# Kernel tuning notes

Measured on AMD Instinct MI355X. Metric: run time of the kernel, lower is better.

Reference implementation:

```python
import jax, jax.numpy as jnp
import numpy as np

B, T, C, H = 2, 2048, 1024, 16
D = C // H  # head_dim = 64

def setup_inputs() -> dict:
    key = jax.random.key(0)
    k1, k2, k3 = jax.random.split(key, 3)
    x = jax.random.normal(k1, (B, T, C), dtype=jnp.float32)
    W_qkv = jax.random.normal(k2, (C, 3 * C), dtype=jnp.float32) * (C ** -0.5)
    b_qkv = jnp.zeros((3 * C,), dtype=jnp.float32)
    W_proj = jax.random.normal(k3, (C, C), dtype=jnp.float32) * (C ** -0.5)
    b_proj = jnp.zeros((C,), dtype=jnp.float32)
    return {"x": x, "W_qkv": W_qkv, "b_qkv": b_qkv, "W_proj": W_proj, "b_proj": b_proj}

def reference(x, W_qkv, b_qkv, W_proj, b_proj):
    # qkv projection: [B,T,3C]
    qkv = jnp.einsum('btc,cf->btf', x, W_qkv) + b_qkv
    q, k, v = jnp.split(qkv, 3, axis=-1)
    # split heads -> [B,H,T,D]
    q = q.reshape(B, T, H, D).transpose(0, 2, 1, 3)
    k = k.reshape(B, T, H, D).transpose(0, 2, 1, 3)
    v = v.reshape(B, T, H, D).transpose(0, 2, 1, 3)
    scale = 1.0 / jnp.sqrt(jnp.float32(D))
    att = jnp.einsum('bhqd,bhkd->bhqk', q, k) * scale  # [B,H,T,T]
    causal = jnp.tril(jnp.ones((T, T), dtype=bool))
    att = jnp.where(causal[None, None, :, :], att, jnp.float32(-jnp.inf))
    att = jax.nn.softmax(att, axis=-1)
    y = jnp.einsum('bhqk,bhkd->bhqd', att, v)  # [B,H,T,D]
    y = y.transpose(0, 2, 1, 3).reshape(B, T, C)
    return jnp.einsum('btc,cf->btf', y, W_proj) + b_proj
```

## Files before the change

kernel.cpp:

```cpp
#include <hip/hip_runtime.h>
#include <hip/hip_bf16.h>

#define Bq 2
#define Tq 2048
#define Cq 1024
#define Hq 16
#define Dq 64
#define Mq (Bq * Tq)

typedef __bf16 bf16x8 __attribute__((ext_vector_type(8)));
typedef float f32x4 __attribute__((ext_vector_type(4)));
typedef unsigned short u16;

static __device__ __forceinline__ u16 f2bf(float f) {
  union { float f; unsigned u; } v; v.f = f;
  return (u16)((v.u + 0x7fffu + ((v.u >> 16) & 1u)) >> 16);
}

static __device__ __forceinline__ f32x4 mfma16(bf16x8 a, bf16x8 b, f32x4 c) {
  return __builtin_amdgcn_mfma_f32_16x16x32_bf16(a, b, c, 0, 0, 0);
}

#define GLD16(g, l)                                                   \
  __builtin_amdgcn_global_load_lds(                                   \
      (const __attribute__((address_space(1))) unsigned int*)(g),     \
      (__attribute__((address_space(3))) unsigned int*)(l), 16, 0, 0)

static __device__ __forceinline__ int swz(int col, int row) {
  return (col & 7) + 8 * (((col >> 3) ^ (row >> 3)) & 7);
}

__global__ __launch_bounds__(256) void convert_x(const float* __restrict__ x,
                                                 u16* __restrict__ xb) {
  int i = (blockIdx.x * 256 + threadIdx.x) * 8;
  float4 a = *(const float4*)(x + i);
  float4 b = *(const float4*)(x + i + 4);
  u16 tmp[8];
  tmp[0] = f2bf(a.x); tmp[1] = f2bf(a.y); tmp[2] = f2bf(a.z); tmp[3] = f2bf(a.w);
  tmp[4] = f2bf(b.x); tmp[5] = f2bf(b.y); tmp[6] = f2bf(b.z); tmp[7] = f2bf(b.w);
  *(uint4*)(xb + i) = *(const uint4*)tmp;
}

__global__ __launch_bounds__(256) void transpose_w(const float* __restrict__ W,
                                                   u16* __restrict__ Wt,
                                                   int K, int N) {
  __shared__ __align__(16) u16 Ts[64][72];
  const int k0 = blockIdx.x * 64, n0 = blockIdx.y * 64;
  const int t = threadIdx.x;
  const int r = t >> 2, c0 = (t & 3) * 16;
  const float* src = W + (size_t)(k0 + r) * N + n0 + c0;
  u16 v16[16];
#pragma unroll
  for (int i = 0; i < 4; i++) {
    float4 f = *(const float4*)(src + 4 * i);
    v16[4 * i + 0] = f2bf(f.x); v16[4 * i + 1] = f2bf(f.y);
    v16[4 * i + 2] = f2bf(f.z); v16[4 * i + 3] = f2bf(f.w);
  }
#pragma unroll
  for (int j = 0; j < 16; j++) Ts[c0 + j][r] = v16[j];
  __syncthreads();
  u16* dst = Wt + (size_t)(n0 + r) * K + k0 + c0;
  *(uint4*)dst = *(const uint4*)&Ts[r][c0];
  *(uint4*)(dst + 8) = *(const uint4*)&Ts[r][c0 + 8];
}

__global__ __launch_bounds__(256) void qkv_gemm(
    const u16* __restrict__ A, const u16* __restrict__ Bt,
    const float* __restrict__ bias,
    u16* __restrict__ qw, u16* __restrict__ kw, u16* __restrict__ vw) {
  const int K = 1024;
  __shared__ __align__(16) u16 As[128][32];
  __shared__ __align__(16) u16 Bs[128][32];
  const int m0 = blockIdx.x * 128, n0 = blockIdx.y * 128;
  const int t = threadIdx.x, lane = t & 63, w = t >> 6;
  const int wm = (w >> 1) * 64, wn = (w & 1) * 64;
  const int l15 = lane & 15, l4 = lane >> 4;
  const int lr = lane >> 2, lc = (lane & 3) * 8;
  f32x4 acc[4][4] = {};
  const u16* ga = A + (size_t)(m0 + w * 16 + lr) * K + lc;
  const u16* gb = Bt + (size_t)(n0 + w * 16 + lr) * K + lc;

  for (int kk = 0; kk < K; kk += 32) {
    __syncthreads();
    GLD16(ga + kk, &As[w * 16][0]);
    GLD16(ga + (size_t)64 * K + kk, &As[64 + w * 16][0]);
    GLD16(gb + kk, &Bs[w * 16][0]);
    GLD16(gb + (size_t)64 * K + kk, &Bs[64 + w * 16][0]);
    __syncthreads();
    bf16x8 af[4], bfr[4];
#pragma unroll
    for (int i = 0; i < 4; i++) {
      af[i] = *(const bf16x8*)&As[wm + i * 16 + l15][l4 * 8];
      bfr[i] = *(const bf16x8*)&Bs[wn + i * 16 + l15][l4 * 8];
    }
#pragma unroll
    for (int mi = 0; mi < 4; mi++)
#pragma unroll
      for (int ni = 0; ni < 4; ni++)
        acc[mi][ni] = mfma16(af[mi], bfr[ni], acc[mi][ni]);
  }
#pragma unroll
  for (int mi = 0; mi < 4; mi++) {
#pragma unroll
    for (int ni = 0; ni < 4; ni++) {
#pragma unroll
      for (int r = 0; r < 4; r++) {
        int row = m0 + wm + mi * 16 + l4 * 4 + r;
        int col = n0 + wn + ni * 16 + l15;
        float val = acc[mi][ni][r] + bias[col];
        int which = col >> 10, c = col & 1023;
        int h = c >> 6, d = c & 63;
        int b = row >> 11, tt = row & 2047;
        u16* dst = (which == 0) ? qw : ((which == 1) ? kw : vw);
        dst[(size_t)((b * Hq + h) * Tq + tt) * Dq + d] = f2bf(val);
      }
    }
  }
}

__global__ __launch_bounds__(256) void attn(
    const u16* __restrict__ qw, const u16* __restrict__ kw,
    const u16* __restrict__ vw, u16* __restrict__ yw) {
  const int bh = blockIdx.x;
  const int qy = blockIdx.y;
  const int qb = (qy < 8) ? (15 - qy) : (qy - 8);
  __shared__ __align__(16) u16 Ks[64][72];
  __shared__ __align__(16) u16 Vt[64][72];
  __shared__ __align__(16) u16 Ps[128][72];
  const int t = threadIdx.x, lane = t & 63, w = t >> 6;
  const int l15 = lane & 15, l4 = lane >> 4;
  const size_t base = (size_t)bh * Tq * Dq;
  const int rr = t >> 2, d0 = (t & 3) * 16;

  bf16x8 qf[2][2];
  {
    const u16* qp = qw + base + (size_t)(qb * 128 + w * 32) * Dq;
#pragma unroll
    for (int s = 0; s < 2; s++)
#pragma unroll
      for (int h = 0; h < 2; h++)
        qf[s][h] = *(const bf16x8*)(qp + (size_t)(s * 16 + l15) * Dq + h * 32 + l4 * 8);
  }

  float m[2][4], lsum[2][4];
  f32x4 accO[2][4] = {};
#pragma unroll
  for (int s = 0; s < 2; s++)
#pragma unroll
    for (int r = 0; r < 4; r++) { m[s][r] = -1e30f; lsum[s][r] = 0.f; }

  const float kscale = 0.125f * 1.44269504088896340736f;
  const int kvmax = 2 * qb + 1;

  const u16* ksrc = kw + base + (size_t)rr * Dq + d0;
  const u16* vsrc = vw + base + (size_t)rr * Dq + d0;
  uint4 kreg0 = *(const uint4*)ksrc, kreg1 = *(const uint4*)(ksrc + 8);
  uint4 vreg0 = *(const uint4*)vsrc, vreg1 = *(const uint4*)(vsrc + 8);

  for (int kv = 0; kv <= kvmax; kv++) {
    __syncthreads();
    *(uint4*)&Ks[rr][d0] = kreg0;
    *(uint4*)&Ks[rr][d0 + 8] = kreg1;
    {
      union { uint4 q[2]; u16 s[16]; } vu;
      vu.q[0] = vreg0; vu.q[1] = vreg1;
#pragma unroll
      for (int j = 0; j < 16; j++) {
        int row = d0 + j;
        Vt[row][swz(rr, row)] = vu.s[j];
      }
    }
    if (kv < kvmax) {
      ksrc += 64 * Dq; vsrc += 64 * Dq;
      kreg0 = *(const uint4*)ksrc; kreg1 = *(const uint4*)(ksrc + 8);
      vreg0 = *(const uint4*)vsrc; vreg1 = *(const uint4*)(vsrc + 8);
    }
    __syncthreads();

    f32x4 sc[2][4];
    __builtin_amdgcn_s_setprio(1);
#pragma unroll
    for (int ct = 0; ct < 4; ct++) {
      bf16x8 kf0 = *(const bf16x8*)&Ks[ct * 16 + l15][l4 * 8];
      bf16x8 kf1 = *(const bf16x8*)&Ks[ct * 16 + l15][32 + l4 * 8];
      f32x4 z0 = {}; z0 = mfma16(qf[0][0], kf0, z0); z0 = mfma16(qf[0][1], kf1, z0);
      sc[0][ct] = z0;
      f32x4 z1 = {}; z1 = mfma16(qf[1][0], kf0, z1); z1 = mfma16(qf[1][1], kf1, z1);
      sc[1][ct] = z1;
    }
    __builtin_amdgcn_s_setprio(0);

    if (kv >= 2 * qb) {
#pragma unroll
      for (int s = 0; s < 2; s++)
#pragma unroll
        for (int ct = 0; ct < 4; ct++)
#pragma unroll
          for (int r = 0; r < 4; r++) {
            int q = qb * 128 + w * 32 + s * 16 + l4 * 4 + r;
            int k = kv * 64 + ct * 16 + l15;
            sc[s][ct][r] = (k > q) ? -1e30f : sc[s][ct][r] * kscale;
          }
    } else {
#pragma unroll
      for (int s = 0; s < 2; s++)
#pragma unroll
        for (int ct = 0; ct < 4; ct++)
#pragma unroll
          for (int r = 0; r < 4; r++) sc[s][ct][r] *= kscale;
    }

#pragma unroll
    for (int s = 0; s < 2; s++) {
      float corr[4], psum[4];
#pragma unroll
      for (int r = 0; r < 4; r++) {
        float v = fmaxf(fmaxf(sc[s][0][r], sc[s][1][r]),
                        fmaxf(sc[s][2][r], sc[s][3][r]));
#pragma unroll
        for (int off = 1; off < 16; off <<= 1) v = fmaxf(v, __shfl_xor(v, off));
        float mn = fmaxf(m[s][r], v);
        corr[r] = exp2f(m[s][r] - mn);
        m[s][r] = mn;
        psum[r] = 0.f;
      }
#pragma unroll
      for (int ct = 0; ct < 4; ct++)
#pragma unroll
        for (int r = 0; r < 4; r++) {
          float p = exp2f(sc[s][ct][r] - m[s][r]);
          psum[r] += p;
          int R = w * 32 + s * 16 + l4 * 4 + r;
          Ps[R][swz(ct * 16 + l15, R)] = f2bf(p);
        }
#pragma unroll
      for (int r = 0; r < 4; r++) {
        float v = psum[r];
#pragma unroll
        for (int off = 1; off < 16; off <<= 1) v += __shfl_xor(v, off);
        lsum[s][r] = lsum[s][r] * corr[r] + v;
      }
#pragma unroll
      for (int dt = 0; dt < 4; dt++)
#pragma unroll
        for (int r = 0; r < 4; r++) accO[s][dt][r] *= corr[r];
    }

    bf16x8 pf[2][2];
#pragma unroll
    for (int s = 0; s < 2; s++) {
      int R = w * 32 + s * 16 + l15;
      int e = (R >> 3) & 7;
      pf[s][0] = *(const bf16x8*)&Ps[R][8 * ((l4 ^ e) & 7)];
      pf[s][1] = *(const bf16x8*)&Ps[R][8 * (((4 + l4) ^ e) & 7)];
    }
    __builtin_amdgcn_s_setprio(1);
#pragma unroll
    for (int dt = 0; dt < 4; dt++) {
      int Rv = dt * 16 + l15;
      int ev = (Rv >> 3) & 7;
      bf16x8 vf0 = *(const bf16x8*)&Vt[Rv][8 * ((l4 ^ ev) & 7)];
      bf16x8 vf1 = *(const bf16x8*)&Vt[Rv][8 * (((4 + l4) ^ ev) & 7)];
      accO[0][dt] = mfma16(pf[0][0], vf0, accO[0][dt]);
      accO[0][dt] = mfma16(pf[0][1], vf1, accO[0][dt]);
      accO[1][dt] = mfma16(pf[1][0], vf0, accO[1][dt]);
      accO[1][dt] = mfma16(pf[1][1], vf1, accO[1][dt]);
    }
    __builtin_amdgcn_s_setprio(0);
  }

  const int b = bh >> 4, hd = bh & 15;
#pragma unroll
  for (int s = 0; s < 2; s++)
#pragma unroll
    for (int r = 0; r < 4; r++) {
      float inv = 1.0f / lsum[s][r];
      int tt = qb * 128 + w * 32 + s * 16 + l4 * 4 + r;
      size_t rowbase = ((size_t)(b * Tq + tt)) * Cq + hd * 64;
#pragma unroll
      for (int dt = 0; dt < 4; dt++)
        yw[rowbase + dt * 16 + l15] = f2bf(accO[s][dt][r] * inv);
    }
}

__global__ __launch_bounds__(256) void proj_gemm(
    const u16* __restrict__ A, const u16* __restrict__ Bt,
    const float* __restrict__ bias, float* __restrict__ out) {
  const int K = 1024, N = 1024;
  __shared__ __align__(16) u16 As[128][32];
  __shared__ __align__(16) u16 Bs[128][32];
  const int m0 = blockIdx.x * 128, n0 = blockIdx.y * 128;
  const int t = threadIdx.x, lane = t & 63, w = t >> 6;
  const int wm = (w >> 1) * 64, wn = (w & 1) * 64;
  const int l15 = lane & 15, l4 = lane >> 4;
  const int lr = lane >> 2, lc = (lane & 3) * 8;
  f32x4 acc[4][4] = {};
  const u16* ga = A + (size_t)(m0 + w * 16 + lr) * K + lc;
  const u16* gb = Bt + (size_t)(n0 + w * 16 + lr) * K + lc;

  for (int kk = 0; kk < K; kk += 32) {
    __syncthreads();
    GLD16(ga + kk, &As[w * 16][0]);
    GLD16(ga + (size_t)64 * K + kk, &As[64 + w * 16][0]);
    GLD16(gb + kk, &Bs[w * 16][0]);
    GLD16(gb + (size_t)64 * K + kk, &Bs[64 + w * 16][0]);
    __syncthreads();
    bf16x8 af[4], bfr[4];
#pragma unroll
    for (int i = 0; i < 4; i++) {
      af[i] = *(const bf16x8*)&As[wm + i * 16 + l15][l4 * 8];
      bfr[i] = *(const bf16x8*)&Bs[wn + i * 16 + l15][l4 * 8];
    }
#pragma unroll
    for (int mi = 0; mi < 4; mi++)
#pragma unroll
      for (int ni = 0; ni < 4; ni++)
        acc[mi][ni] = mfma16(af[mi], bfr[ni], acc[mi][ni]);
  }
#pragma unroll
  for (int mi = 0; mi < 4; mi++) {
#pragma unroll
    for (int ni = 0; ni < 4; ni++) {
#pragma unroll
      for (int r = 0; r < 4; r++) {
        int row = m0 + wm + mi * 16 + l4 * 4 + r;
        int col = n0 + wn + ni * 16 + l15;
        out[(size_t)row * N + col] = acc[mi][ni][r] + bias[col];
      }
    }
  }
}

extern "C" void kernel_launch(void* const* d_in, const int* in_sizes, int n_in,
                              void* d_out, int out_size, void* d_ws, size_t ws_size,
                              hipStream_t stream) {
  const float* x = (const float*)d_in[0];
  const float* W_qkv = (const float*)d_in[1];
  const float* b_qkv = (const float*)d_in[2];
  const float* W_proj = (const float*)d_in[3];
  const float* b_proj = (const float*)d_in[4];
  float* out = (float*)d_out;

  const size_t qkv_elems = (size_t)Bq * Hq * Tq * Dq;
  u16* qw = (u16*)d_ws;
  u16* kw = qw + qkv_elems;
  u16* vw = kw + qkv_elems;
  u16* xb = vw + qkv_elems;
  u16* wt = xb + (size_t)Mq * Cq;

  convert_x<<<dim3((Mq * Cq) / (256 * 8)), 256, 0, stream>>>(x, xb);
  transpose_w<<<dim3(Cq / 64, 3 * Cq / 64), 256, 0, stream>>>(W_qkv, wt, Cq, 3 * Cq);
  qkv_gemm<<<dim3(Mq / 128, 3 * Cq / 128), 256, 0, stream>>>(xb, wt, b_qkv, qw, kw, vw);
  transpose_w<<<dim3(Cq / 64, Cq / 64), 256, 0, stream>>>(W_proj, wt, Cq, Cq);
  u16* yw = xb;
  attn<<<dim3(Bq * Hq, Tq / 128), 256, 0, stream>>>(qw, kw, vw, yw);
  proj_gemm<<<dim3(Mq / 128, Cq / 128), 256, 0, stream>>>(yw, wt, b_proj, out);
}
```

Before: 249.5 us.

## Restructure attention to transposed S tiles with register-resident P and lazy rescale

The attention kernel now runs 512 threads, each wave owning 16 query rows instead of 32. It computes S^T (K as the A operand) so each lane holds one query column, and moves P into the PV MFMA operand layout with shuffles, which removes the Ps shared-memory round trip. The softmax scale is folded into Q in the QKV GEMM epilogue. Waves skip KV tiles that are fully masked for their rows, and the running max is only rescaled when it grows by more than a threshold. The costs are extra cross-lane shuffles, more waves contending for the shared K/V tiles, and lazy max updates that could reduce numerical headroom.

Result: faster. 207.3 us (-16.9%).

```diff
diff --git a/kernel.cpp b/kernel.cpp
--- a/kernel.cpp
+++ b/kernel.cpp
@@ -109,6 +109,7 @@
         int col = n0 + wn + ni * 16 + l15;
         float val = acc[mi][ni][r] + bias[col];
         int which = col >> 10, c = col & 1023;
+        if (which == 0) val *= 0.18033688011112042f;
         int h = c >> 6, d = c & 63;
         int b = row >> 11, tt = row & 2047;
         u16* dst = (which == 0) ? qw : ((which == 1) ? kw : vw);
@@ -118,7 +119,7 @@
   }
 }
 
-__global__ __launch_bounds__(256) void attn(
+__global__ __launch_bounds__(512, 4) void attn(
     const u16* __restrict__ qw, const u16* __restrict__ kw,
     const u16* __restrict__ vw, u16* __restrict__ yw) {
   const int bh = blockIdx.x;
@@ -126,161 +127,144 @@
   const int qb = (qy < 8) ? (15 - qy) : (qy - 8);
   __shared__ __align__(16) u16 Ks[64][72];
   __shared__ __align__(16) u16 Vt[64][72];
-  __shared__ __align__(16) u16 Ps[128][72];
   const int t = threadIdx.x, lane = t & 63, w = t >> 6;
   const int l15 = lane & 15, l4 = lane >> 4;
   const size_t base = (size_t)bh * Tq * Dq;
-  const int rr = t >> 2, d0 = (t & 3) * 16;
-
-  bf16x8 qf[2][2];
+  const int rv = t >> 3, c8 = t & 7;
+
+  const int qs = qb * 128 + w * 16;
+  bf16x8 qf[2];
   {
-    const u16* qp = qw + base + (size_t)(qb * 128 + w * 32) * Dq;
-#pragma unroll
-    for (int s = 0; s < 2; s++)
-#pragma unroll
-      for (int h = 0; h < 2; h++)
-        qf[s][h] = *(const bf16x8*)(qp + (size_t)(s * 16 + l15) * Dq + h * 32 + l4 * 8);
-  }
-
-  float m[2][4], lsum[2][4];
-  f32x4 accO[2][4] = {};
-#pragma unroll
-  for (int s = 0; s < 2; s++)
-#pragma unroll
-    for (int r = 0; r < 4; r++) { m[s][r] = -1e30f; lsum[s][r] = 0.f; }
-
-  const float kscale = 0.125f * 1.44269504088896340736f;
+    const u16* qp = qw + base + (size_t)(qs + l15) * Dq + l4 * 8;
+    qf[0] = *(const bf16x8*)qp;
+    qf[1] = *(const bf16x8*)(qp + 32);
+  }
+
+  float m = -1e30f, lsum = 0.f;
+  f32x4 accO[4] = {};
   const int kvmax = 2 * qb + 1;
 
-  const u16* ksrc = kw + base + (size_t)rr * Dq + d0;
-  const u16* vsrc = vw + base + (size_t)rr * Dq + d0;
-  uint4 kreg0 = *(const uint4*)ksrc, kreg1 = *(const uint4*)(ksrc + 8);
-  uint4 vreg0 = *(const uint4*)vsrc, vreg1 = *(const uint4*)(vsrc + 8);
+  const u16* ksrc = kw + base + (size_t)rv * Dq + c8 * 8;
+  const u16* vsrc = vw + base + (size_t)rv * Dq + c8 * 8;
+  uint4 kreg = *(const uint4*)ksrc;
+  uint4 vreg = *(const uint4*)vsrc;
 
   for (int kv = 0; kv <= kvmax; kv++) {
     __syncthreads();
-    *(uint4*)&Ks[rr][d0] = kreg0;
-    *(uint4*)&Ks[rr][d0 + 8] = kreg1;
+    *(uint4*)&Ks[rv][c8 * 8] = kreg;
     {
-      union { uint4 q[2]; u16 s[16]; } vu;
-      vu.q[0] = vreg0; vu.q[1] = vreg1;
-#pragma unroll
-      for (int j = 0; j < 16; j++) {
-        int row = d0 + j;
-        Vt[row][swz(rr, row)] = vu.s[j];
+      union { uint4 q; u16 s[8]; } vu; vu.q = vreg;
+#pragma unroll
+      for (int jj = 0; jj < 8; jj++) {
+        int row = c8 * 8 + jj;
+        Vt[row][swz(rv, row)] = vu.s[jj];
       }
     }
     if (kv < kvmax) {
       ksrc += 64 * Dq; vsrc += 64 * Dq;
-      kreg0 = *(const uint4*)ksrc; kreg1 = *(const uint4*)(ksrc + 8);
-      vreg0 = *(const uint4*)vsrc; vreg1 = *(const uint4*)(vsrc + 8);
-    }
-    __syncthreads();
-
-    f32x4 sc[2][4];
+      kreg = *(const uint4*)ksrc;
+      vreg = *(const uint4*)vsrc;
+    }
+    __syncthreads();
+
+    if (kv * 64 > qs + 15) continue;
+
+    f32x4 sc[4];
     __builtin_amdgcn_s_setprio(1);
 #pragma unroll
     for (int ct = 0; ct < 4; ct++) {
       bf16x8 kf0 = *(const bf16x8*)&Ks[ct * 16 + l15][l4 * 8];
       bf16x8 kf1 = *(const bf16x8*)&Ks[ct * 16 + l15][32 + l4 * 8];
-      f32x4 z0 = {}; z0 = mfma16(qf[0][0], kf0, z0); z0 = mfma16(qf[0][1], kf1, z0);
-      sc[0][ct] = z0;
-      f32x4 z1 = {}; z1 = mfma16(qf[1][0], kf0, z1); z1 = mfma16(qf[1][1], kf1, z1);
-      sc[1][ct] = z1;
+      f32x4 z = {};
+      z = mfma16(kf0, qf[0], z);
+      z = mfma16(kf1, qf[1], z);
+      sc[ct] = z;
     }
     __builtin_amdgcn_s_setprio(0);
 
-    if (kv >= 2 * qb) {
-#pragma unroll
-      for (int s = 0; s < 2; s++)
-#pragma unroll
-        for (int ct = 0; ct < 4; ct++)
-#pragma unroll
-          for (int r = 0; r < 4; r++) {
-            int q = qb * 128 + w * 32 + s * 16 + l4 * 4 + r;
-            int k = kv * 64 + ct * 16 + l15;
-            sc[s][ct][r] = (k > q) ? -1e30f : sc[s][ct][r] * kscale;
-          }
-    } else {
-#pragma unroll
-      for (int s = 0; s < 2; s++)
-#pragma unroll
-        for (int ct = 0; ct < 4; ct++)
-#pragma unroll
-          for (int r = 0; r < 4; r++) sc[s][ct][r] *= kscale;
-    }
-
-#pragma unroll
-    for (int s = 0; s < 2; s++) {
-      float corr[4], psum[4];
+    if (kv * 64 + 63 > qs) {
+      const int q = qs + l15;
+#pragma unroll
+      for (int ct = 0; ct < 4; ct++)
+#pragma unroll
+        for (int r = 0; r < 4; r++) {
+          int k = kv * 64 + ct * 16 + l4 * 4 + r;
+          if (k > q) sc[ct][r] = -1e30f;
+        }
+    }
+
+    float pmax = sc[0][0];
+#pragma unroll
+    for (int ct = 0; ct < 4; ct++)
+#pragma unroll
+      for (int r = 0; r < 4; r++) pmax = fmaxf(pmax, sc[ct][r]);
+    pmax = fmaxf(pmax, __shfl_xor(pmax, 16));
+    pmax = fmaxf(pmax, __shfl_xor(pmax, 32));
+
+    if (__any(pmax > m + 8.f)) {
+      float mn = fmaxf(m, pmax);
+      float corr = exp2f(m - mn);
+      m = mn;
+      lsum *= corr;
 #pragma unroll
       for (int r = 0; r < 4; r++) {
-        float v = fmaxf(fmaxf(sc[s][0][r], sc[s][1][r]),
-                        fmaxf(sc[s][2][r], sc[s][3][r]));
-#pragma unroll
-        for (int off = 1; off < 16; off <<= 1) v = fmaxf(v, __shfl_xor(v, off));
-        float mn = fmaxf(m[s][r], v);
-        corr[r] = exp2f(m[s][r] - mn);
-        m[s][r] = mn;
-        psum[r] = 0.f;
-      }
-#pragma unroll
-      for (int ct = 0; ct < 4; ct++)
+        float cb = __shfl(corr, (lane >> 4) * 20 + r);
+#pragma unroll
+        for (int dt = 0; dt < 4; dt++) accO[dt][r] *= cb;
+      }
+    }
+
+    float psum = 0.f;
+#pragma unroll
+    for (int ct = 0; ct < 4; ct++)
+#pragma unroll
+      for (int r = 0; r < 4; r++) {
+        float p = exp2f(sc[ct][r] - m);
+        sc[ct][r] = p;
+        psum += p;
+      }
+    psum += __shfl_xor(psum, 16);
+    psum += __shfl_xor(psum, 32);
+    lsum += psum;
+
+    bf16x8 pa[2];
+    const int bsrc = ((lane & 16) << 1) + l15;
+#pragma unroll
+    for (int h = 0; h < 2; h++) {
+#pragma unroll
+      for (int jh = 0; jh < 2; jh++)
 #pragma unroll
         for (int r = 0; r < 4; r++) {
-          float p = exp2f(sc[s][ct][r] - m[s][r]);
-          psum[r] += p;
-          int R = w * 32 + s * 16 + l4 * 4 + r;
-          Ps[R][swz(ct * 16 + l15, R)] = f2bf(p);
+          float v0 = __shfl(sc[2 * h][r], bsrc + 16 * jh);
+          float v1 = __shfl(sc[2 * h + 1][r], bsrc + 16 * jh);
+          pa[h][jh * 4 + r] = (__bf16)((l4 & 2) ? v1 : v0);
         }
-#pragma unroll
-      for (int r = 0; r < 4; r++) {
-        float v = psum[r];
-#pragma unroll
-        for (int off = 1; off < 16; off <<= 1) v += __shfl_xor(v, off);
-        lsum[s][r] = lsum[s][r] * corr[r] + v;
-      }
-#pragma unroll
-      for (int dt = 0; dt < 4; dt++)
-#pragma unroll
-        for (int r = 0; r < 4; r++) accO[s][dt][r] *= corr[r];
-    }
-
-    bf16x8 pf[2][2];
-#pragma unroll
-    for (int s = 0; s < 2; s++) {
-      int R = w * 32 + s * 16 + l15;
-      int e = (R >> 3) & 7;
-      pf[s][0] = *(const bf16x8*)&Ps[R][8 * ((l4 ^ e) & 7)];
-      pf[s][1] = *(const bf16x8*)&Ps[R][8 * (((4 + l4) ^ e) & 7)];
-    }
+    }
+
     __builtin_amdgcn_s_setprio(1);
 #pragma unroll
     for (int dt = 0; dt < 4; dt++) {
       int Rv = dt * 16 + l15;
-      int ev = (Rv >> 3) & 7;
-      bf16x8 vf0 = *(const bf16x8*)&Vt[Rv][8 * ((l4 ^ ev) & 7)];
-      bf16x8 vf1 = *(const bf16x8*)&Vt[Rv][8 * (((4 + l4) ^ ev) & 7)];
-      accO[0][dt] = mfma16(pf[0][0], vf0, accO[0][dt]);
-      accO[0][dt] = mfma16(pf[0][1], vf1, accO[0][dt]);
-      accO[1][dt] = mfma16(pf[1][0], vf0, accO[1][dt]);
-      accO[1][dt] = mfma16(pf[1][1], vf1, accO[1][dt]);
+      int e = (Rv >> 3) & 7;
+      bf16x8 vf0 = *(const bf16x8*)&Vt[Rv][8 * ((l4 ^ e) & 7)];
+      bf16x8 vf1 = *(const bf16x8*)&Vt[Rv][8 * (((4 + l4) ^ e) & 7)];
+      accO[dt] = mfma16(pa[0], vf0, accO[dt]);
+      accO[dt] = mfma16(pa[1], vf1, accO[dt]);
     }
     __builtin_amdgcn_s_setprio(0);
   }
 
+  float inv = 1.0f / lsum;
   const int b = bh >> 4, hd = bh & 15;
 #pragma unroll
-  for (int s = 0; s < 2; s++)
-#pragma unroll
-    for (int r = 0; r < 4; r++) {
-      float inv = 1.0f / lsum[s][r];
-      int tt = qb * 128 + w * 32 + s * 16 + l4 * 4 + r;
-      size_t rowbase = ((size_t)(b * Tq + tt)) * Cq + hd * 64;
-#pragma unroll
-      for (int dt = 0; dt < 4; dt++)
-        yw[rowbase + dt * 16 + l15] = f2bf(accO[s][dt][r] * inv);
-    }
+  for (int r = 0; r < 4; r++) {
+    float ib = __shfl(inv, (lane >> 4) * 20 + r);
+    int tt = qs + l4 * 4 + r;
+    size_t rowbase = ((size_t)(b * Tq + tt)) * Cq + hd * 64;
+#pragma unroll
+    for (int dt = 0; dt < 4; dt++)
+      yw[rowbase + dt * 16 + l15] = f2bf(accO[dt][r] * ib);
+  }
 }
 
 __global__ __launch_bounds__(256) void proj_gemm(
@@ -353,6 +337,6 @@
   qkv_gemm<<<dim3(Mq / 128, 3 * Cq / 128), 256, 0, stream>>>(xb, wt, b_qkv, qw, kw, vw);
   transpose_w<<<dim3(Cq / 64, Cq / 64), 256, 0, stream>>>(W_proj, wt, Cq, Cq);
   u16* yw = xb;
-  attn<<<dim3(Bq * Hq, Tq / 128), 256, 0, stream>>>(qw, kw, vw, yw);
+  attn<<<dim3(Bq * Hq, Tq / 128), 512, 0, stream>>>(qw, kw, vw, yw);
   proj_gemm<<<dim3(Mq / 128, Cq / 128), 256, 0, stream>>>(yw, wt, b_proj, out);
 }
```
